# Performance work log

Hardware: AMD Instinct MI355X
Metric: run time of the kernel (lower is better)

Reference implementation:

```python
import jax, jax.numpy as jnp
import numpy as np

MEX_C = 2.0 / (np.sqrt(3.0) * np.pi ** 0.25)

def mexican_hat(z):
    return MEX_C * (z * z - 1.0) * jnp.exp(-0.5 * z * z)

def setup_inputs() -> dict:
    key = jax.random.key(0)
    ks = jax.random.split(key, 5)
    B, T, D, O = 4, 2048, 128, 128
    x = jax.random.normal(ks[0], (B, T, D), dtype=jnp.float32)
    # init like torch: scale ~ U(0.5,1.5), translation ~ U(-0.5,0.5), kaiming-ish weights
    scale = jax.random.uniform(ks[1], (O, D), dtype=jnp.float32, minval=0.5, maxval=1.5)
    translation = jax.random.uniform(ks[2], (O, D), dtype=jnp.float32, minval=-0.5, maxval=0.5)
    bound = 1.0 / np.sqrt(D)
    wavelet_weights = jax.random.uniform(ks[3], (O, D), dtype=jnp.float32, minval=-bound, maxval=bound)
    base_w = jax.random.uniform(ks[4], (O, D), dtype=jnp.float32, minval=-bound, maxval=bound)
    ln_gamma = jnp.ones((D,), dtype=jnp.float32)
    ln_beta = jnp.zeros((D,), dtype=jnp.float32)
    return {"x": x, "scale": scale, "translation": translation,
            "wavelet_weights": wavelet_weights, "base_w": base_w,
            "ln_gamma": ln_gamma, "ln_beta": ln_beta}

def reference(x, scale, translation, wavelet_weights, base_w, ln_gamma, ln_beta):
    B, T, D = x.shape
    O = wavelet_weights.shape[0]
    # LayerNorm over last dim (eps = 1e-5, torch default)
    mu = jnp.mean(x, axis=-1, keepdims=True)
    var = jnp.mean((x - mu) ** 2, axis=-1, keepdims=True)
    x_norm = (x - mu) / jnp.sqrt(var + 1e-5) * ln_gamma + ln_beta
    x_flat = x_norm.reshape(B * T, D)                      # (N, D)
    s = jax.nn.softplus(scale) + 0.1                       # (O, D)
    # broadcast intermediate (N, O, D) — the memory-bound path
    z = (x_flat[:, None, :] - translation[None]) / s[None]
    w = jnp.clip(mexican_hat(z), -10.0, 10.0)              # (N, O, D)
    wavelet_out = jnp.einsum('nod,od->no', w, wavelet_weights)
    base_out = x.reshape(B * T, D) @ base_w.T              # base uses raw x
    out = wavelet_out + jax.nn.silu(base_out)
    return out.reshape(B, T, O)
```

## Files before the change

### kernel.cpp

```cpp
#include <hip/hip_runtime.h>


#define D_DIM 128
#define O_DIM 128
#define ROWS  16
#define BLOCK 512

#define C1     0.72134752f
#define SQRT_C 0.84932180f
#define WWK    1.2023651f
#define LOG2E  1.44269504f

__global__ __launch_bounds__(256) void wavekan_prep(
    const float* __restrict__ scale,
    const float* __restrict__ trans,
    const float* __restrict__ ww,
    const float* __restrict__ bw,
    float4* __restrict__ wsW)
{
    int idx = blockIdx.x * blockDim.x + threadIdx.x;
    if (idx >= O_DIM * D_DIM) return;
    int o = idx >> 7;
    int d = idx & (D_DIM - 1);
    float sc = scale[idx];
    float sp = fmaxf(sc, 0.0f) + log1pf(__expf(-fabsf(sc)));
    float is2 = SQRT_C / (sp + 0.1f);
    float4 w;
    w.x = trans[idx] * is2;
    w.y = is2;
    w.z = ww[idx] * WWK;
    w.w = bw[idx];
    wsW[d * O_DIM + o] = w;
}

template<bool USE_WS>
__global__ __launch_bounds__(BLOCK, 4) void wavekan_main(
    const float* __restrict__ x,
    const float* __restrict__ scale,
    const float* __restrict__ trans,
    const float* __restrict__ ww,
    const float* __restrict__ bw,
    const float* __restrict__ gamma,
    const float* __restrict__ beta,
    const float4* __restrict__ wsW,
    float* __restrict__ out,
    int N)
{
    __shared__ float2 s_lr[ROWS * D_DIM];

    const int tid  = threadIdx.x;
    const int row0 = blockIdx.x * ROWS;

    {
        const int r  = tid >> 5;
        const int j  = tid & 31;
        const int d0 = j * 4;
        const int grow = row0 + r;

        float4 v4 = make_float4(0.f, 0.f, 0.f, 0.f);
        if (grow < N)
            v4 = *reinterpret_cast<const float4*>(x + (size_t)grow * D_DIM + d0);
        float v[4] = {v4.x, v4.y, v4.z, v4.w};

        float sum = 0.0f, ssq = 0.0f;
        #pragma unroll
        for (int k = 0; k < 4; ++k) { sum += v[k]; ssq += v[k] * v[k]; }
        #pragma unroll
        for (int m = 1; m < 32; m <<= 1) {
            sum += __shfl_xor(sum, m, 64);
            ssq += __shfl_xor(ssq, m, 64);
        }
        const float mean = sum * (1.0f / D_DIM);
        const float var  = ssq * (1.0f / D_DIM) - mean * mean;
        const float rstd = rsqrtf(var + 1e-5f);

        float4 g4 = *reinterpret_cast<const float4*>(gamma + d0);
        float4 b4 = *reinterpret_cast<const float4*>(beta + d0);
        float g[4] = {g4.x, g4.y, g4.z, g4.w};
        float b[4] = {b4.x, b4.y, b4.z, b4.w};

        #pragma unroll
        for (int k = 0; k < 4; ++k) {
            float lnv = (v[k] - mean) * rstd * g[k] + b[k];
            s_lr[r * D_DIM + d0 + k] = make_float2(lnv, v[k]);
        }
    }
    __syncthreads();

    const int o = tid & (O_DIM - 1);
    const int g = tid >> 7;
    const float2* __restrict__ lr = s_lr + g * 4 * D_DIM;

    float accw[4] = {0.f, 0.f, 0.f, 0.f};
    float accb[4] = {0.f, 0.f, 0.f, 0.f};

    #pragma unroll 2
    for (int d = 0; d < D_DIM; ++d) {
        float tws, is, wwk, bwv;
        if (USE_WS) {
            float4 w = wsW[d * O_DIM + o];
            tws = w.x; is = w.y; wwk = w.z; bwv = w.w;
        } else {
            int idx = o * D_DIM + d;
            float sc = scale[idx];
            float sp = fmaxf(sc, 0.0f) + log1pf(__expf(-fabsf(sc)));
            is  = SQRT_C / (sp + 0.1f);
            tws = trans[idx] * is;
            wwk = ww[idx] * WWK;
            bwv = bw[idx];
        }
        #pragma unroll
        for (int k = 0; k < 4; ++k) {
            float2 v = lr[k * D_DIM + d];
            float u  = fmaf(v.x, is, -tws);
            float u2 = u * u;
            float e  = __builtin_amdgcn_exp2f(-u2);
            accw[k]  = fmaf((u2 - C1) * e, wwk, accw[k]);
            accb[k]  = fmaf(v.y, bwv, accb[k]);
        }
    }

    #pragma unroll
    for (int k = 0; k < 4; ++k) {
        const int rr = row0 + g * 4 + k;
        if (rr < N) {
            float bsum = accb[k];
            float sig  = 1.0f / (1.0f + __builtin_amdgcn_exp2f(-LOG2E * bsum));
            out[(size_t)rr * O_DIM + o] = accw[k] + bsum * sig;
        }
    }
}

extern "C" void kernel_launch(void* const* d_in, const int* in_sizes, int n_in,
                              void* d_out, int out_size, void* d_ws, size_t ws_size,
                              hipStream_t stream) {
    const float* x     = (const float*)d_in[0];
    const float* scale = (const float*)d_in[1];
    const float* trans = (const float*)d_in[2];
    const float* ww    = (const float*)d_in[3];
    const float* bw    = (const float*)d_in[4];
    const float* gamma = (const float*)d_in[5];
    const float* beta  = (const float*)d_in[6];
    float* out = (float*)d_out;

    const int N = in_sizes[0] / D_DIM;
    const int grid = (N + ROWS - 1) / ROWS;

    const size_t ws_needed = (size_t)O_DIM * D_DIM * sizeof(float4);
    if (ws_size >= ws_needed) {
        wavekan_prep<<<(O_DIM * D_DIM + 255) / 256, 256, 0, stream>>>(
            scale, trans, ww, bw, (float4*)d_ws);
        wavekan_main<true><<<grid, BLOCK, 0, stream>>>(
            x, scale, trans, ww, bw, gamma, beta, (const float4*)d_ws, out, N);
    } else {
        wavekan_main<false><<<grid, BLOCK, 0, stream>>>(
            x, scale, trans, ww, bw, gamma, beta, nullptr, out, N);
    }
}
```

Baseline: 99.40 us.

## Use 1024-thread blocks with two rows per thread and prefetch weights

The block size doubles to 1024 threads with 16 rows per block. Each thread now computes 2 output rows instead of 4, and LayerNorm uses 64 lanes per row. The workspace weight loop software-prefetches the next d's float4 weights one iteration ahead. The aim is more parallelism and better hiding of global load latency, at the cost of half the weight reuse per load (twice the weight traffic per row) and larger blocks.

```diff
diff --git a/kernel.cpp b/kernel.cpp
--- a/kernel.cpp
+++ b/kernel.cpp
@@ -4,7 +4,7 @@
 #define D_DIM 128
 #define O_DIM 128
 #define ROWS  16
-#define BLOCK 512
+#define BLOCK 1024
 
 #define C1     0.72134752f
 #define SQRT_C 0.84932180f
@@ -34,7 +34,7 @@
 }
 
 template<bool USE_WS>
-__global__ __launch_bounds__(BLOCK, 4) void wavekan_main(
+__global__ __launch_bounds__(BLOCK, 8) void wavekan_main(
     const float* __restrict__ x,
     const float* __restrict__ scale,
     const float* __restrict__ trans,
@@ -52,21 +52,19 @@
     const int row0 = blockIdx.x * ROWS;
 
     {
-        const int r  = tid >> 5;
-        const int j  = tid & 31;
-        const int d0 = j * 4;
+        const int r  = tid >> 6;
+        const int j  = tid & 63;
+        const int d0 = j * 2;
         const int grow = row0 + r;
 
-        float4 v4 = make_float4(0.f, 0.f, 0.f, 0.f);
+        float2 v2 = make_float2(0.f, 0.f);
         if (grow < N)
-            v4 = *reinterpret_cast<const float4*>(x + (size_t)grow * D_DIM + d0);
-        float v[4] = {v4.x, v4.y, v4.z, v4.w};
+            v2 = *reinterpret_cast<const float2*>(x + (size_t)grow * D_DIM + d0);
 
-        float sum = 0.0f, ssq = 0.0f;
+        float sum = v2.x + v2.y;
+        float ssq = v2.x * v2.x + v2.y * v2.y;
         #pragma unroll
-        for (int k = 0; k < 4; ++k) { sum += v[k]; ssq += v[k] * v[k]; }
-        #pragma unroll
-        for (int m = 1; m < 32; m <<= 1) {
+        for (int m = 1; m < 64; m <<= 1) {
             sum += __shfl_xor(sum, m, 64);
             ssq += __shfl_xor(ssq, m, 64);
         }
@@ -74,59 +72,71 @@
         const float var  = ssq * (1.0f / D_DIM) - mean * mean;
         const float rstd = rsqrtf(var + 1e-5f);
 
-        float4 g4 = *reinterpret_cast<const float4*>(gamma + d0);
-        float4 b4 = *reinterpret_cast<const float4*>(beta + d0);
-        float g[4] = {g4.x, g4.y, g4.z, g4.w};
-        float b[4] = {b4.x, b4.y, b4.z, b4.w};
+        float2 g2 = *reinterpret_cast<const float2*>(gamma + d0);
+        float2 b2 = *reinterpret_cast<const float2*>(beta + d0);
 
-        #pragma unroll
-        for (int k = 0; k < 4; ++k) {
-            float lnv = (v[k] - mean) * rstd * g[k] + b[k];
-            s_lr[r * D_DIM + d0 + k] = make_float2(lnv, v[k]);
-        }
+        s_lr[r * D_DIM + d0]     = make_float2((v2.x - mean) * rstd * g2.x + b2.x, v2.x);
+        s_lr[r * D_DIM + d0 + 1] = make_float2((v2.y - mean) * rstd * g2.y + b2.y, v2.y);
     }
     __syncthreads();
 
     const int o = tid & (O_DIM - 1);
     const int g = tid >> 7;
-    const float2* __restrict__ lr = s_lr + g * 4 * D_DIM;
+    const float2* __restrict__ lr = s_lr + g * 2 * D_DIM;
 
-    float accw[4] = {0.f, 0.f, 0.f, 0.f};
-    float accb[4] = {0.f, 0.f, 0.f, 0.f};
+    float accw0 = 0.f, accw1 = 0.f, accb0 = 0.f, accb1 = 0.f;
 
-    #pragma unroll 2
-    for (int d = 0; d < D_DIM; ++d) {
-        float tws, is, wwk, bwv;
-        if (USE_WS) {
-            float4 w = wsW[d * O_DIM + o];
-            tws = w.x; is = w.y; wwk = w.z; bwv = w.w;
-        } else {
+    if (USE_WS) {
+        float4 w = wsW[o];
+        #pragma unroll 4
+        for (int d = 0; d < D_DIM; ++d) {
+            float4 wn = wsW[(((d + 1) & (D_DIM - 1)) << 7) + o];
+            float2 v0 = lr[d];
+            float2 v1 = lr[D_DIM + d];
+
+            float u0 = fmaf(v0.x, w.y, -w.x);
+            float u1 = fmaf(v1.x, w.y, -w.x);
+            float q0 = u0 * u0;
+            float q1 = u1 * u1;
+            float e0 = __builtin_amdgcn_exp2f(-q0);
+            float e1 = __builtin_amdgcn_exp2f(-q1);
+            accw0 = fmaf((q0 - C1) * e0, w.z, accw0);
+            accw1 = fmaf((q1 - C1) * e1, w.z, accw1);
+            accb0 = fmaf(v0.y, w.w, accb0);
+            accb1 = fmaf(v1.y, w.w, accb1);
+            w = wn;
+        }
+    } else {
+        for (int d = 0; d < D_DIM; ++d) {
             int idx = o * D_DIM + d;
             float sc = scale[idx];
             float sp = fmaxf(sc, 0.0f) + log1pf(__expf(-fabsf(sc)));
-            is  = SQRT_C / (sp + 0.1f);
-            tws = trans[idx] * is;
-            wwk = ww[idx] * WWK;
-            bwv = bw[idx];
-        }
-        #pragma unroll
-        for (int k = 0; k < 4; ++k) {
-            float2 v = lr[k * D_DIM + d];
-            float u  = fmaf(v.x, is, -tws);
-            float u2 = u * u;
-            float e  = __builtin_amdgcn_exp2f(-u2);
-            accw[k]  = fmaf((u2 - C1) * e, wwk, accw[k]);
-            accb[k]  = fmaf(v.y, bwv, accb[k]);
+            float is  = SQRT_C / (sp + 0.1f);
+            float tws = trans[idx] * is;
+            float wwk = ww[idx] * WWK;
+            float bwv = bw[idx];
+            float2 v0 = lr[d];
+            float2 v1 = lr[D_DIM + d];
+            float u0 = fmaf(v0.x, is, -tws);
+            float u1 = fmaf(v1.x, is, -tws);
+            float q0 = u0 * u0;
+            float q1 = u1 * u1;
+            accw0 = fmaf((q0 - C1) * __builtin_amdgcn_exp2f(-q0), wwk, accw0);
+            accw1 = fmaf((q1 - C1) * __builtin_amdgcn_exp2f(-q1), wwk, accw1);
+            accb0 = fmaf(v0.y, bwv, accb0);
+            accb1 = fmaf(v1.y, bwv, accb1);
         }
     }
 
-    #pragma unroll
-    for (int k = 0; k < 4; ++k) {
-        const int rr = row0 + g * 4 + k;
-        if (rr < N) {
-            float bsum = accb[k];
-            float sig  = 1.0f / (1.0f + __builtin_amdgcn_exp2f(-LOG2E * bsum));
-            out[(size_t)rr * O_DIM + o] = accw[k] + bsum * sig;
+    {
+        const int rr0 = row0 + g * 2;
+        if (rr0 < N) {
+            float sig0 = 1.0f / (1.0f + __builtin_amdgcn_exp2f(-LOG2E * accb0));
+            out[(size_t)rr0 * O_DIM + o] = accw0 + accb0 * sig0;
+        }
+        if (rr0 + 1 < N) {
+            float sig1 = 1.0f / (1.0f + __builtin_amdgcn_exp2f(-LOG2E * accb1));
+            out[(size_t)(rr0 + 1) * O_DIM + o] = accw1 + accb1 * sig1;
         }
     }
 }
```

New measurement: 104.0 us. 1.05x slower.
